# Performance work log

Hardware: AMD Instinct MI355X
Metric: run time of the kernel (lower is better)

Reference implementation:

```python
import jax, jax.numpy as jnp
import numpy as np

NQ = 4          # number of qubits (hardcoded in the original module)
LET = 'pqrs'    # einsum letters for the 4 qubit axes


def setup_inputs() -> dict:
    key = jax.random.key(0)
    k1, k2 = jax.random.split(key)
    B = 1048576  # 2^20 samples
    x = jax.random.normal(k1, (B, NQ), dtype=jnp.float32)          # RX angles per sample
    weights = jax.random.normal(k2, (3, NQ, 3), dtype=jnp.float32) * 0.1  # (layers, wires, 3)
    return {"x": x, "weights": weights}


def _apply_1q(state, U, w):
    # state: (B,2,2,2,2) complex, U: (2,2) complex, applied on wire w
    sub = 'b' + LET
    out = sub.replace(LET[w], 'x')
    return jnp.einsum(f'x{LET[w]},{sub}->{out}', U, state)


def _cnot(state, c, t):
    # CNOT control c -> target t: flip target axis on the control=1 half
    s0, s1 = jnp.split(state, 2, axis=1 + c)
    s1 = jnp.flip(s1, axis=1 + t)
    return jnp.concatenate([s0, s1], axis=1 + c)


def _rot(phi, theta, omega):
    # PennyLane Rot(phi, theta, omega) = RZ(omega) RY(theta) RZ(phi)
    c = jnp.cos(theta * 0.5)
    s = jnp.sin(theta * 0.5)
    m00 = jnp.exp(-0.5j * (phi + omega)) * c
    m01 = -jnp.exp(0.5j * (phi - omega)) * s
    m10 = jnp.exp(-0.5j * (phi - omega)) * s
    m11 = jnp.exp(0.5j * (phi + omega)) * c
    return jnp.stack([jnp.stack([m00, m01]), jnp.stack([m10, m11])]).astype(jnp.complex64)


def _forward(x, weights):
    # --- RX(x_i) on |0>^4: product state, built as an outer product ---
    c = jnp.cos(x * 0.5)
    s = jnp.sin(x * 0.5)
    mi = np.complex64(-1j)
    vs = [jnp.stack([c[:, i].astype(jnp.complex64), mi * s[:, i]], axis=-1) for i in range(NQ)]
    state = jnp.einsum('bp,bq,br,bs->bpqrs', *vs)  # (B,2,2,2,2) complex64

    # --- StronglyEntanglingLayers (default ranges r = l % (NQ-1) + 1) ---
    n_layers = weights.shape[0]
    for l in range(n_layers):
        for i in range(NQ):
            U = _rot(weights[l, i, 0], weights[l, i, 1], weights[l, i, 2])
            state = _apply_1q(state, U, i)
        r = (l % (NQ - 1)) + 1
        for i in range(NQ):
            state = _cnot(state, i, (i + r) % NQ)

    # --- <Z_i> expectation values ---
    probs = state.real ** 2 + state.imag ** 2  # (B,2,2,2,2) float32
    outs = []
    for w in range(NQ):
        axes = tuple(a for a in range(1, NQ + 1) if a != w + 1)
        m = probs.sum(axis=axes)  # (B,2) marginal over wire w
        outs.append(m[:, 0] - m[:, 1])
    return jnp.stack(outs, axis=-1)  # (B, NQ)


def reference(x, weights):
    return _forward(x, weights)
```

## Files before the change

### kernel.cpp

```cpp
#include <hip/hip_runtime.h>
#include <hip/hip_bf16.h>


__global__ void build_C_kernel(const float* __restrict__ w, float4* __restrict__ C) {
    __shared__ float Vr[16][16];
    __shared__ float Vi[16][16];
    __shared__ float A[4][16][16];

    const int tid = threadIdx.x;

    if (tid < 16) {
        const int k = tid;
        float ar[16], ai[16];
#pragma unroll
        for (int j = 0; j < 16; ++j) { ar[j] = (j == k) ? 1.f : 0.f; ai[j] = 0.f; }

#pragma unroll
        for (int l = 0; l < 3; ++l) {
#pragma unroll
            for (int i = 0; i < 4; ++i) {
                float phi = w[l * 12 + i * 3 + 0];
                float th  = w[l * 12 + i * 3 + 1];
                float om  = w[l * 12 + i * 3 + 2];
                float ct = cosf(0.5f * th), st = sinf(0.5f * th);
                float alpha = 0.5f * (phi + om), beta = 0.5f * (phi - om);
                float sa, ca, sb, cb;
                sincosf(alpha, &sa, &ca);
                sincosf(beta,  &sb, &cb);
                float m00r =  ca * ct, m00i = -sa * ct;
                float m01r = -cb * st, m01i = -sb * st;
                float m10r =  cb * st, m10i = -sb * st;
                float m11r =  ca * ct, m11i =  sa * ct;
                int mask = 1 << i;
#pragma unroll
                for (int j = 0; j < 16; ++j) {
                    if (j & mask) continue;
                    int j1 = j | mask;
                    float a0r = ar[j],  a0i = ai[j];
                    float a1r = ar[j1], a1i = ai[j1];
                    ar[j]  = m00r * a0r - m00i * a0i + m01r * a1r - m01i * a1i;
                    ai[j]  = m00r * a0i + m00i * a0r + m01r * a1i + m01i * a1r;
                    ar[j1] = m10r * a0r - m10i * a0i + m11r * a1r - m11i * a1i;
                    ai[j1] = m10r * a0i + m10i * a0r + m11r * a1i + m11i * a1r;
                }
            }
            int r = (l % 3) + 1;
#pragma unroll
            for (int i = 0; i < 4; ++i) {
                int c = i, t = (i + r) & 3;
                int cm = 1 << c, tm = 1 << t;
#pragma unroll
                for (int j = 0; j < 16; ++j) {
                    if ((j & cm) && !(j & tm)) {
                        int j2 = j | tm;
                        float tr = ar[j], ti = ai[j];
                        ar[j] = ar[j2]; ai[j] = ai[j2];
                        ar[j2] = tr;    ai[j2] = ti;
                    }
                }
            }
        }

        int p = __popc(k) & 3;
        float pr = (p == 0) ? 1.f : (p == 2) ? -1.f : 0.f;
        float pi = (p == 1) ? -1.f : (p == 3) ? 1.f : 0.f;
#pragma unroll
        for (int j = 0; j < 16; ++j) {
            Vr[j][k] = ar[j] * pr - ai[j] * pi;
            Vi[j][k] = ar[j] * pi + ai[j] * pr;
        }
    }
    __syncthreads();

    {
        const int k = tid >> 4, l = tid & 15;
        float acc0 = 0.f, acc1 = 0.f, acc2 = 0.f, acc3 = 0.f;
#pragma unroll
        for (int j = 0; j < 16; ++j) {
            float p = Vr[j][k] * Vr[j][l] + Vi[j][k] * Vi[j][l];
            acc0 += (j & 1) ? -p : p;
            acc1 += (j & 2) ? -p : p;
            acc2 += (j & 4) ? -p : p;
            acc3 += (j & 8) ? -p : p;
        }
        A[0][k][l] = acc0; A[1][k][l] = acc1; A[2][k][l] = acc2; A[3][k][l] = acc3;
    }
    __syncthreads();

    if (tid < 81) {
        int d[4];
        d[0] = tid % 3; d[1] = (tid / 3) % 3; d[2] = (tid / 9) % 3; d[3] = tid / 27;
        float acc0 = 0.f, acc1 = 0.f, acc2 = 0.f, acc3 = 0.f;
#pragma unroll
        for (int o = 0; o < 16; ++o) {
            int k = 0, l = 0; float sign = 1.f;
#pragma unroll
            for (int q = 0; q < 4; ++q) {
                int oq = (o >> q) & 1;
                if (d[q] == 2) { k |= oq << q; l |= (1 - oq) << q; }
                else {
                    k |= oq << q; l |= oq << q;
                    if (d[q] == 1 && oq == 1) sign = -sign;
                }
            }
            acc0 += sign * A[0][k][l];
            acc1 += sign * A[1][k][l];
            acc2 += sign * A[2][k][l];
            acc3 += sign * A[3][k][l];
        }
        const float inv16 = 0.0625f;
        C[tid] = make_float4(acc0 * inv16, acc1 * inv16, acc2 * inv16, acc3 * inv16);
    }
}

#define SPT 4
#define BLOCK 256

template <bool GUARD>
__launch_bounds__(BLOCK)
__global__ void qlayer_kernel(const float* __restrict__ x,
                              const float4* __restrict__ Cg,
                              float* __restrict__ out, int B) {
    __shared__ float4 C[81];
    if (threadIdx.x < 81) C[threadIdx.x] = Cg[threadIdx.x];
    __syncthreads();

    const int base = blockIdx.x * (BLOCK * SPT) + threadIdx.x;

    float c0[SPT], s0[SPT], c3[SPT], s3[SPT];
    float G9[SPT][9];
    float z[SPT][4];

#pragma unroll
    for (int s = 0; s < SPT; ++s) {
        int idx = base + s * BLOCK;
        float4 xv;
        if (!GUARD || idx < B) xv = ((const float4*)x)[idx];
        else xv = make_float4(0.f, 0.f, 0.f, 0.f);

        float c1, s1, c2, s2;
        __sincosf(xv.x, &s0[s], &c0[s]);
        __sincosf(xv.y, &s1, &c1);
        __sincosf(xv.z, &s2, &c2);
        __sincosf(xv.w, &s3[s], &c3[s]);

        G9[s][0] = 1.f;     G9[s][1] = c1;      G9[s][2] = s1;
        G9[s][3] = c2;      G9[s][4] = c1 * c2; G9[s][5] = s1 * c2;
        G9[s][6] = s2;      G9[s][7] = c1 * s2; G9[s][8] = s1 * s2;

        z[s][0] = z[s][1] = z[s][2] = z[s][3] = 0.f;
    }

#pragma unroll
    for (int t3 = 0; t3 < 3; ++t3) {
#pragma unroll
        for (int i9 = 0; i9 < 9; ++i9) {
            const int combo = i9 + 9 * t3;
            const float4 Ca = C[combo * 3 + 0];
            const float4 Cb = C[combo * 3 + 1];
            const float4 Cc = C[combo * 3 + 2];
#pragma unroll
            for (int s = 0; s < SPT; ++s) {
                float g = G9[s][i9];
                if (t3 == 1) g *= c3[s];
                if (t3 == 2) g *= s3[s];
                float r0 = fmaf(c0[s], Cb.x, fmaf(s0[s], Cc.x, Ca.x));
                float r1 = fmaf(c0[s], Cb.y, fmaf(s0[s], Cc.y, Ca.y));
                float r2 = fmaf(c0[s], Cb.z, fmaf(s0[s], Cc.z, Ca.z));
                float r3 = fmaf(c0[s], Cb.w, fmaf(s0[s], Cc.w, Ca.w));
                z[s][0] = fmaf(g, r0, z[s][0]);
                z[s][1] = fmaf(g, r1, z[s][1]);
                z[s][2] = fmaf(g, r2, z[s][2]);
                z[s][3] = fmaf(g, r3, z[s][3]);
            }
        }
    }

#pragma unroll
    for (int s = 0; s < SPT; ++s) {
        int idx = base + s * BLOCK;
        if (!GUARD || idx < B) {
            float4 o; o.x = z[s][0]; o.y = z[s][1]; o.z = z[s][2]; o.w = z[s][3];
            ((float4*)out)[idx] = o;
        }
    }
}

extern "C" void kernel_launch(void* const* d_in, const int* in_sizes, int n_in,
                              void* d_out, int out_size, void* d_ws, size_t ws_size,
                              hipStream_t stream) {
    const float* x = (const float*)d_in[0];
    const float* w = (const float*)d_in[1];
    float* out = (float*)d_out;
    float4* C = (float4*)d_ws;

    int B = in_sizes[0] / 4;

    build_C_kernel<<<1, 256, 0, stream>>>(w, C);

    const int spb = BLOCK * SPT;
    if (B % spb == 0) {
        qlayer_kernel<false><<<B / spb, BLOCK, 0, stream>>>(x, C, out, B);
    } else {
        qlayer_kernel<true><<<(B + spb - 1) / spb, BLOCK, 0, stream>>>(x, C, out, B);
    }
}
```

Measured before the change: 92.17 us.

## Fuse coefficient build into main kernel, recomputing per block

Removes the separate single-block build_C launch and has every block of the main kernel rebuild the 81-entry coefficient table in shared memory. Gate matrices are computed once per gate by 12 threads with fast __sincosf, replacing per-thread precise sincos. This drops one kernel launch and the serial dependency between the two kernels. In exchange, every one of the 1024 blocks repeats the simulation and contraction and adds several barriers before its main work, which raises per-block latency and lowers accuracy through the fast intrinsics.

Measured after the change: 94.44 us. 2.5% more time.

```diff
diff --git a/kernel.cpp b/kernel.cpp
--- a/kernel.cpp
+++ b/kernel.cpp
@@ -2,12 +2,36 @@
 #include <hip/hip_bf16.h>
 
 
-__global__ void build_C_kernel(const float* __restrict__ w, float4* __restrict__ C) {
+#define SPT 4
+#define BLOCK 256
+
+template <bool GUARD>
+__launch_bounds__(BLOCK)
+__global__ void qlayer_kernel(const float* __restrict__ x,
+                              const float* __restrict__ w,
+                              float* __restrict__ out, int B) {
+    __shared__ float Gm[12][8];
     __shared__ float Vr[16][16];
     __shared__ float Vi[16][16];
     __shared__ float A[4][16][16];
+    __shared__ float4 C[81];
 
     const int tid = threadIdx.x;
+
+    if (tid < 12) {
+        float phi = w[tid * 3 + 0];
+        float th  = w[tid * 3 + 1];
+        float om  = w[tid * 3 + 2];
+        float ct, st, sa, ca, sb, cb;
+        __sincosf(0.5f * th, &st, &ct);
+        __sincosf(0.5f * (phi + om), &sa, &ca);
+        __sincosf(0.5f * (phi - om), &sb, &cb);
+        Gm[tid][0] =  ca * ct;  Gm[tid][1] = -sa * ct;
+        Gm[tid][2] = -cb * st;  Gm[tid][3] = -sb * st;
+        Gm[tid][4] =  cb * st;  Gm[tid][5] = -sb * st;
+        Gm[tid][6] =  ca * ct;  Gm[tid][7] =  sa * ct;
+    }
+    __syncthreads();
 
     if (tid < 16) {
         const int k = tid;
@@ -19,18 +43,11 @@
         for (int l = 0; l < 3; ++l) {
 #pragma unroll
             for (int i = 0; i < 4; ++i) {
-                float phi = w[l * 12 + i * 3 + 0];
-                float th  = w[l * 12 + i * 3 + 1];
-                float om  = w[l * 12 + i * 3 + 2];
-                float ct = cosf(0.5f * th), st = sinf(0.5f * th);
-                float alpha = 0.5f * (phi + om), beta = 0.5f * (phi - om);
-                float sa, ca, sb, cb;
-                sincosf(alpha, &sa, &ca);
-                sincosf(beta,  &sb, &cb);
-                float m00r =  ca * ct, m00i = -sa * ct;
-                float m01r = -cb * st, m01i = -sb * st;
-                float m10r =  cb * st, m10i = -sb * st;
-                float m11r =  ca * ct, m11i =  sa * ct;
+                const int g = l * 4 + i;
+                float m00r = Gm[g][0], m00i = Gm[g][1];
+                float m01r = Gm[g][2], m01i = Gm[g][3];
+                float m10r = Gm[g][4], m10i = Gm[g][5];
+                float m11r = Gm[g][6], m11i = Gm[g][7];
                 int mask = 1 << i;
 #pragma unroll
                 for (int j = 0; j < 16; ++j) {
@@ -88,8 +105,8 @@
     __syncthreads();
 
     if (tid < 81) {
-        int d[4];
-        d[0] = tid % 3; d[1] = (tid / 3) % 3; d[2] = (tid / 9) % 3; d[3] = tid / 27;
+        int d0 = tid % 3, d1 = (tid / 3) % 3, d2 = (tid / 9) % 3, d3 = tid / 27;
+        int d[4] = {d0, d1, d2, d3};
         float acc0 = 0.f, acc1 = 0.f, acc2 = 0.f, acc3 = 0.f;
 #pragma unroll
         for (int o = 0; o < 16; ++o) {
@@ -111,21 +128,9 @@
         const float inv16 = 0.0625f;
         C[tid] = make_float4(acc0 * inv16, acc1 * inv16, acc2 * inv16, acc3 * inv16);
     }
-}
-
-#define SPT 4
-#define BLOCK 256
-
-template <bool GUARD>
-__launch_bounds__(BLOCK)
-__global__ void qlayer_kernel(const float* __restrict__ x,
-                              const float4* __restrict__ Cg,
-                              float* __restrict__ out, int B) {
-    __shared__ float4 C[81];
-    if (threadIdx.x < 81) C[threadIdx.x] = Cg[threadIdx.x];
-    __syncthreads();
-
-    const int base = blockIdx.x * (BLOCK * SPT) + threadIdx.x;
+    __syncthreads();
+
+    const int base = blockIdx.x * (BLOCK * SPT) + tid;
 
     float c0[SPT], s0[SPT], c3[SPT], s3[SPT];
     float G9[SPT][9];
@@ -144,9 +149,9 @@
         __sincosf(xv.z, &s2, &c2);
         __sincosf(xv.w, &s3[s], &c3[s]);
 
-        G9[s][0] = 1.f;     G9[s][1] = c1;      G9[s][2] = s1;
-        G9[s][3] = c2;      G9[s][4] = c1 * c2; G9[s][5] = s1 * c2;
-        G9[s][6] = s2;      G9[s][7] = c1 * s2; G9[s][8] = s1 * s2;
+        G9[s][0] = 1.f;  G9[s][1] = c1;      G9[s][2] = s1;
+        G9[s][3] = c2;   G9[s][4] = c1 * c2; G9[s][5] = s1 * c2;
+        G9[s][6] = s2;   G9[s][7] = c1 * s2; G9[s][8] = s1 * s2;
 
         z[s][0] = z[s][1] = z[s][2] = z[s][3] = 0.f;
     }
@@ -192,16 +197,13 @@
     const float* x = (const float*)d_in[0];
     const float* w = (const float*)d_in[1];
     float* out = (float*)d_out;
-    float4* C = (float4*)d_ws;
 
     int B = in_sizes[0] / 4;
-
-    build_C_kernel<<<1, 256, 0, stream>>>(w, C);
 
     const int spb = BLOCK * SPT;
     if (B % spb == 0) {
-        qlayer_kernel<false><<<B / spb, BLOCK, 0, stream>>>(x, C, out, B);
+        qlayer_kernel<false><<<B / spb, BLOCK, 0, stream>>>(x, w, out, B);
     } else {
-        qlayer_kernel<true><<<(B + spb - 1) / spb, BLOCK, 0, stream>>>(x, C, out, B);
+        qlayer_kernel<true><<<(B + spb - 1) / spb, BLOCK, 0, stream>>>(x, w, out, B);
     }
 }
```
